# Performance work log

Hardware: AMD Instinct MI355X
Metric: run time of the kernel (lower is better)

The kernel has to match this reference:

```python
import jax, jax.numpy as jnp
import numpy as np
from jax import lax

D_MODEL = 768
BATCH = 16
SEQ = 2048
N_BLOCKS = D_MODEL // 3
LN_EPS = 1e-5


def setup_inputs() -> dict:
    key = jax.random.key(0)
    ks = jax.random.split(key, 4)
    scale = 1.0 / np.sqrt(D_MODEL)
    x = jax.random.normal(ks[0], (BATCH, SEQ, D_MODEL), dtype=jnp.float32)
    W_biv = jax.random.normal(ks[1], (D_MODEL, D_MODEL), dtype=jnp.float32) * scale
    b_biv = jnp.zeros((D_MODEL,), dtype=jnp.float32)
    W_decay = jax.random.normal(ks[2], (1, D_MODEL), dtype=jnp.float32) * scale
    b_decay = jnp.full((1,), 1.4, dtype=jnp.float32)  # nn.init.constant_(decay_proj.bias, 1.4)
    W_in = jax.random.normal(ks[3], (D_MODEL, D_MODEL), dtype=jnp.float32) * scale
    b_in = jnp.zeros((D_MODEL,), dtype=jnp.float32)
    ln_gamma = jnp.ones((D_MODEL,), dtype=jnp.float32)
    ln_beta = jnp.zeros((D_MODEL,), dtype=jnp.float32)
    return {"x": x, "W_biv": W_biv, "b_biv": b_biv, "W_decay": W_decay,
            "b_decay": b_decay, "W_in": W_in, "b_in": b_in,
            "ln_gamma": ln_gamma, "ln_beta": ln_beta}


def _quat_rotate_blocks(h_blocks, biv):
    """h_blocks, biv: (batch, n_blocks, 3) -> rotated (batch, n_blocks, 3)."""
    norm_b = jnp.maximum(jnp.linalg.norm(biv, axis=-1, keepdims=True), 1e-8)
    half = norm_b * 0.5
    w = jnp.cos(half)[..., 0]
    s = (jnp.sin(half) / norm_b)[..., 0]
    # note the original maps bivector components in reversed order
    qx = s * biv[..., 2]
    qy = -s * biv[..., 1]
    qz = s * biv[..., 0]
    vx, vy, vz = h_blocks[..., 0], h_blocks[..., 1], h_blocks[..., 2]
    tx = 2.0 * (qy * vz - qz * vy)
    ty = 2.0 * (qz * vx - qx * vz)
    tz = 2.0 * (qx * vy - qy * vx)
    rx = vx + w * tx + (qy * tz - qz * ty)
    ry = vy + w * ty + (qz * tx - qx * tz)
    rz = vz + w * tz + (qx * ty - qy * tx)
    return jnp.stack([rx, ry, rz], axis=-1)


def reference(x, W_biv, b_biv, W_decay, b_decay, W_in, b_in, ln_gamma, ln_beta):
    B, S, D = x.shape
    nb = D // 3
    # precompute all per-timestep projections as big GEMMs
    biv = (jnp.einsum('bsd,ed->bse', x, W_biv) + b_biv).reshape(B, S, nb, 3)
    decay = jax.nn.sigmoid(jnp.einsum('bsd,ed->bse', x, W_decay) + b_decay)  # (B,S,1)
    inj = jnp.einsum('bsd,ed->bse', x, W_in) + b_in  # (B,S,D)

    def step(h, t):
        biv_t, decay_t, inj_t = t
        rot = _quat_rotate_blocks(h.reshape(B, nb, 3), biv_t).reshape(B, D)
        h_next = decay_t * rot + inj_t
        return h_next, h_next

    xs = (jnp.moveaxis(biv, 1, 0), jnp.moveaxis(decay, 1, 0), jnp.moveaxis(inj, 1, 0))
    h0 = jnp.zeros((B, D), dtype=x.dtype)
    _, out = lax.scan(step, h0, xs)  # (S,B,D)
    out = jnp.moveaxis(out, 0, 1)  # (B,S,D)

    mean = jnp.mean(out, axis=-1, keepdims=True)
    var = jnp.mean(jnp.square(out - mean), axis=-1, keepdims=True)
    normed = (out - mean) * lax.rsqrt(var + LN_EPS) * ln_gamma + ln_beta
    return normed + x
```

## Files before the change

kernel.cpp:

```cpp
#include <hip/hip_runtime.h>
#include <stdint.h>

#define D_MODEL 768
#define BATCH   16
#define SEQ     2048
#define M_ROWS  (BATCH * SEQ)
#define LN_EPS  1e-5f

#define CHUNKS  64
#define CLEN    (SEQ / CHUNKS)
#define PFB     8

typedef __attribute__((ext_vector_type(4))) float        f32x4;
typedef __attribute__((ext_vector_type(8))) __bf16       bf16x8;
typedef __attribute__((ext_vector_type(2))) unsigned int u32x2;

__device__ __forceinline__ unsigned short f2bf(float f) {
    union { float f; uint32_t u; } v; v.f = f;
    uint32_t u = v.u;
    uint32_t r = (u + 0x7FFFu + ((u >> 16) & 1u)) >> 16;
    return (unsigned short)r;
}
__device__ __forceinline__ float bf2f(unsigned short u) {
    union { uint32_t u; float f; } v; v.u = (uint32_t)u << 16; return v.f;
}
__device__ __forceinline__ float bfx(u32x2 v, int k) {
    unsigned int w = (k & 2) ? v[1] : v[0];
    return bf2f((unsigned short)(w >> ((k & 1) * 16)));
}

__device__ __forceinline__ void gload_lds16(const void* g, void* l) {
    __builtin_amdgcn_global_load_lds(
        (const __attribute__((address_space(1))) unsigned int*)g,
        (__attribute__((address_space(3))) unsigned int*)l,
        16, 0, 0);
}

__global__ __launch_bounds__(256) void k_conv_decay(
    const float* __restrict__ x, const float* __restrict__ Wd,
    const float* __restrict__ bd, unsigned short* __restrict__ xb,
    float* __restrict__ decay)
{
    int row = blockIdx.x;
    int i   = threadIdx.x;
    const float* xr = x + (size_t)row * D_MODEL;
    float v0 = xr[i], v1 = xr[i + 256], v2 = xr[i + 512];
    unsigned short* xbr = xb + (size_t)row * D_MODEL;
    xbr[i] = f2bf(v0); xbr[i + 256] = f2bf(v1); xbr[i + 512] = f2bf(v2);

    float part = v0 * Wd[i] + v1 * Wd[i + 256] + v2 * Wd[i + 512];
    #pragma unroll
    for (int off = 32; off; off >>= 1) part += __shfl_down(part, off);
    __shared__ float wsum[4];
    int wid = i >> 6, lane = i & 63;
    if (lane == 0) wsum[wid] = part;
    __syncthreads();
    if (i == 0) {
        float s = wsum[0] + wsum[1] + wsum[2] + wsum[3] + bd[0];
        decay[row] = 1.f / (1.f + __expf(-s));
    }
}

__global__ __launch_bounds__(256) void k_conv_w(
    const float* __restrict__ Wb, const float* __restrict__ Wi,
    unsigned short* __restrict__ Wdst)
{
    const int NW = D_MODEL * D_MODEL;
    int g = blockIdx.x * 256 + threadIdx.x;
    int base = g * 4;
    unsigned short* dst = Wdst + base;
    const float* src;
    if (base < NW) { src = Wb + base; }
    else           { src = Wi + (base - NW); }
    float4 v = *(const float4*)src;
    ushort4 o;
    o.x = f2bf(v.x); o.y = f2bf(v.y); o.z = f2bf(v.z); o.w = f2bf(v.w);
    *(ushort4*)dst = o;
}

#define BM 128
#define BN 128
#define NBX 12

__global__ __launch_bounds__(256) void k_gemm_fused(
    const unsigned short* __restrict__ A,
    const unsigned short* __restrict__ Bw,
    const float* __restrict__ bias_biv, const float* __restrict__ bias_in,
    u32x2* __restrict__ bivq, u32x2* __restrict__ injq)
{
    const int K = D_MODEL;
    __shared__ unsigned short As[BM * 32];
    __shared__ unsigned short Bs[BN * 32];

    int id  = blockIdx.x;
    int swz = (id & 7) * (NBX * (M_ROWS / BM) / 8) + (id >> 3);
    int bxc = swz % NBX, byr = swz / NBX;
    int m0 = byr * BM, n0 = bxc * BN;

    int tid  = threadIdx.x;
    int wave = tid >> 6, lane = tid & 63;
    int wm = wave >> 1, wn = wave & 1;

    f32x4 acc[4][4] = {};

    for (int k0 = 0; k0 < K; k0 += 32) {
        #pragma unroll
        for (int hh = 0; hh < 2; ++hh) {
            int c  = wave * 128 + hh * 64 + lane;
            int r  = c >> 2;
            int sl = (c & 3) ^ ((r >> 1) & 3);
            gload_lds16(A  + (size_t)(m0 + r) * K + k0 + sl * 8, (char*)As + c * 16);
            gload_lds16(Bw + (size_t)(n0 + r) * K + k0 + sl * 8, (char*)Bs + c * 16);
        }
        __syncthreads();

        bf16x8 af[4], bfr[4];
        int kq = lane >> 4;
        int rl = lane & 15;
        #pragma unroll
        for (int i = 0; i < 4; ++i) {
            int ra = wm * 64 + i * 16 + rl;
            int ca = kq ^ ((ra >> 1) & 3);
            af[i]  = *reinterpret_cast<const bf16x8*>((const char*)As + ra * 64 + ca * 16);
            int rb = wn * 64 + i * 16 + rl;
            int cb = kq ^ ((rb >> 1) & 3);
            bfr[i] = *reinterpret_cast<const bf16x8*>((const char*)Bs + rb * 64 + cb * 16);
        }
        #pragma unroll
        for (int i = 0; i < 4; ++i)
            #pragma unroll
            for (int j = 0; j < 4; ++j)
                acc[i][j] = __builtin_amdgcn_mfma_f32_16x16x32_bf16(af[i], bfr[j], acc[i][j], 0, 0, 0);
        __syncthreads();
    }

    u32x2* Cq; const float* bias; int nloc;
    if (n0 < D_MODEL) { Cq = bivq; bias = bias_biv; nloc = n0; }
    else              { Cq = injq; bias = bias_in;  nloc = n0 - D_MODEL; }
    int cl = lane & 15;
    int q4 = lane >> 4;
    int rowq0 = (m0 + wm * 64) >> 2;
    #pragma unroll
    for (int j = 0; j < 4; ++j) {
        int col = nloc + wn * 64 + j * 16 + cl;
        float bs = bias[col];
        #pragma unroll
        for (int i = 0; i < 4; ++i) {
            f32x4 a = acc[i][j];
            unsigned int lo = (unsigned int)f2bf(a[0] + bs) | ((unsigned int)f2bf(a[1] + bs) << 16);
            unsigned int hi = (unsigned int)f2bf(a[2] + bs) | ((unsigned int)f2bf(a[3] + bs) << 16);
            size_t qi = (size_t)(rowq0 + i * 4 + q4) * D_MODEL + col;
            u32x2 pk = {lo, hi};
            Cq[qi] = pk;
        }
    }
}

#define QSTEP_CORE(BX,BY,BZ, IX,IY,IZ, DD)                              \
    {   float n2   = (BX)*(BX) + (BY)*(BY) + (BZ)*(BZ);                 \
        float nrm  = fmaxf(__builtin_sqrtf(n2), 1e-8f);                 \
        float half = 0.5f * nrm;                                        \
        float w = __cosf(half);                                         \
        float s = __sinf(half) / nrm;                                   \
        float qx = s * (BZ), qy = -s * (BY), qz = s * (BX);             \
        float tx = 2.f * (qy * hz - qz * hy);                           \
        float ty = 2.f * (qz * hx - qx * hz);                           \
        float tz = 2.f * (qx * hy - qy * hx);                           \
        float rx = hx + w * tx + (qy * tz - qz * ty);                   \
        float ry = hy + w * ty + (qz * tx - qx * tz);                   \
        float rz = hz + w * tz + (qx * ty - qy * tx);                   \
        hx = fmaf((DD), rx, (IX));                                      \
        hy = fmaf((DD), ry, (IY));                                      \
        hz = fmaf((DD), rz, (IZ));                                      \
        float nQw = w * Qw - qx * Qx - qy * Qy - qz * Qz;               \
        float nQx = w * Qx + Qw * qx + (qy * Qz - qz * Qy);             \
        float nQy = w * Qy + Qw * qy + (qz * Qx - qx * Qz);             \
        float nQz = w * Qz + Qw * qz + (qx * Qy - qy * Qx);             \
        Qw = nQw; Qx = nQx; Qy = nQy; Qz = nQz;                         \
        S *= (DD);                                                      \
    }

__global__ __launch_bounds__(256) void k_scan_p1(
    const u32x2* __restrict__ bivq, const u32x2* __restrict__ injq,
    const float* __restrict__ decay,
    float* __restrict__ ops)
{
    int j = threadIdx.x;
    int c = blockIdx.x & (CHUNKS - 1);
    int b = blockIdx.x >> 6;
    size_t qrow = ((size_t)b * SEQ + (size_t)c * CLEN) >> 2;
    const u32x2* bv = bivq + qrow * D_MODEL + 3 * j;
    const u32x2* ij = injq + qrow * D_MODEL + 3 * j;
    const float* dk = decay + (size_t)b * SEQ + c * CLEN;

    u32x2 Ab0, Ab1, Ab2, Ai0, Ai1, Ai2; f32x4 Ad;
    u32x2 Bb0, Bb1, Bb2, Bi0, Bi1, Bi2; f32x4 Bd;

    #define LOADQ1(P, q)                                                  \
        P##b0 = bv[(size_t)(q) * D_MODEL + 0];                            \
        P##b1 = bv[(size_t)(q) * D_MODEL + 1];                            \
        P##b2 = bv[(size_t)(q) * D_MODEL + 2];                            \
        P##i0 = ij[(size_t)(q) * D_MODEL + 0];                            \
        P##i1 = ij[(size_t)(q) * D_MODEL + 1];                            \
        P##i2 = ij[(size_t)(q) * D_MODEL + 2];                            \
        P##d  = *(const f32x4*)(dk + (q) * 4);

    #define PROC41(P)                                                     \
        _Pragma("unroll")                                                 \
        for (int k = 0; k < 4; ++k) {                                     \
            float bx = bfx(P##b0, k), by = bfx(P##b1, k), bz = bfx(P##b2, k); \
            float ix = bfx(P##i0, k), iy = bfx(P##i1, k), iz = bfx(P##i2, k); \
            float d = P##d[k];                                            \
            QSTEP_CORE(bx, by, bz, ix, iy, iz, d)                         \
        }

    float hx = 0.f, hy = 0.f, hz = 0.f;
    float Qw = 1.f, Qx = 0.f, Qy = 0.f, Qz = 0.f, S = 1.f;

    LOADQ1(A, 0)
    LOADQ1(B, 1)
    #pragma unroll
    for (int q0 = 0; q0 < CLEN / 4; q0 += 2) {
        PROC41(A)
        if (q0 + 2 < CLEN / 4) { LOADQ1(A, q0 + 2) }
        PROC41(B)
        if (q0 + 3 < CLEN / 4) { LOADQ1(B, q0 + 3) }
    }
    #undef LOADQ1
    #undef PROC41

    float* op = ops + ((size_t)(b * CHUNKS + c) * 256 + j) * 8;
    f32x4 o0 = {Qw, Qx, Qy, Qz};
    f32x4 o1 = {S, hx, hy, hz};
    *(f32x4*)op = o0;
    *(f32x4*)(op + 4) = o1;
}

__global__ __launch_bounds__(64) void k_scan_p2(
    const float* __restrict__ ops, float* __restrict__ hs)
{
    int gid = blockIdx.x * 64 + threadIdx.x;
    int j = gid & 255, b = gid >> 8;

    float q0[PFB], q1[PFB], q2[PFB], q3[PFB], sc[PFB], o0[PFB], o1[PFB], o2[PFB];
    #pragma unroll
    for (int p = 0; p < PFB; ++p) {
        const float* op = ops + ((size_t)(b * CHUNKS + p) * 256 + j) * 8;
        f32x4 a = *(const f32x4*)op, bb = *(const f32x4*)(op + 4);
        q0[p] = a[0]; q1[p] = a[1]; q2[p] = a[2]; q3[p] = a[3];
        sc[p] = bb[0]; o0[p] = bb[1]; o1[p] = bb[2]; o2[p] = bb[3];
    }
    float hx = 0.f, hy = 0.f, hz = 0.f;
    for (int c0 = 0; c0 < CHUNKS; c0 += PFB) {
        #pragma unroll
        for (int p = 0; p < PFB; ++p) {
            int c = c0 + p;
            float* h = hs + ((size_t)(b * CHUNKS + c) * 256 + j) * 3;
            h[0] = hx; h[1] = hy; h[2] = hz;
            float w = q0[p], qx = q1[p], qy = q2[p], qz = q3[p];
            float s = sc[p], bx = o0[p], by = o1[p], bz = o2[p];
            int cn = c + PFB;
            if (cn < CHUNKS) {
                const float* op = ops + ((size_t)(b * CHUNKS + cn) * 256 + j) * 8;
                f32x4 a = *(const f32x4*)op, bb = *(const f32x4*)(op + 4);
                q0[p] = a[0]; q1[p] = a[1]; q2[p] = a[2]; q3[p] = a[3];
                sc[p] = bb[0]; o0[p] = bb[1]; o1[p] = bb[2]; o2[p] = bb[3];
            }
            float tx = 2.f * (qy * hz - qz * hy);
            float ty = 2.f * (qz * hx - qx * hz);
            float tz = 2.f * (qx * hy - qy * hx);
            float rx = hx + w * tx + (qy * tz - qz * ty);
            float ry = hy + w * ty + (qz * tx - qx * tz);
            float rz = hz + w * tz + (qx * ty - qy * tx);
            hx = fmaf(s, rx, bx);
            hy = fmaf(s, ry, by);
            hz = fmaf(s, rz, bz);
        }
    }
}

__global__ __launch_bounds__(256) void k_scan_p3(
    const u32x2* __restrict__ bivq, const u32x2* __restrict__ injq,
    const float* __restrict__ decay, const float* __restrict__ hs,
    const float* __restrict__ x, const float* __restrict__ gamma,
    const float* __restrict__ beta, float* __restrict__ out)
{
    int blk = blockIdx.x;
    int c = blk & (CHUNKS - 1);
    int b = blk >> 6;
    int j = threadIdx.x;
    size_t rowbase = ((size_t)b * SEQ + (size_t)c * CLEN) * D_MODEL + (size_t)j * 3;
    size_t qrow    = ((size_t)b * SEQ + (size_t)c * CLEN) >> 2;
    const u32x2* bv = bivq + qrow * D_MODEL + 3 * j;
    const u32x2* ij = injq + qrow * D_MODEL + 3 * j;
    const float* xr = x   + rowbase;
    float*       po = out + rowbase;
    const float* dk = decay + (size_t)b * SEQ + c * CLEN;
    const float* h0 = hs + ((size_t)(b * CHUNKS + c) * 256 + j) * 3;
    float hx = h0[0], hy = h0[1], hz = h0[2];
    float Qw = 1.f, Qx = 0.f, Qy = 0.f, Qz = 0.f, S = 1.f;

    float g0 = gamma[j * 3], g1 = gamma[j * 3 + 1], g2 = gamma[j * 3 + 2];
    float e0 = beta[j * 3],  e1 = beta[j * 3 + 1],  e2 = beta[j * 3 + 2];

    __shared__ float sb[8];
    __shared__ float mv[2];
    int wid = j >> 6, lane = j & 63;

    u32x2 Ab0, Ab1, Ab2, Ai0, Ai1, Ai2; f32x4 Ad;
    float Ax0, Ax1, Ax2, Ax3, Ax4, Ax5, Ax6, Ax7, Ax8, Ax9, Ax10, Ax11;
    u32x2 Bb0, Bb1, Bb2, Bi0, Bi1, Bi2; f32x4 Bd;
    float Bx0, Bx1, Bx2, Bx3, Bx4, Bx5, Bx6, Bx7, Bx8, Bx9, Bx10, Bx11;

    #define LOADQ3(P, q)                                                  \
        P##b0 = bv[(size_t)(q) * D_MODEL + 0];                            \
        P##b1 = bv[(size_t)(q) * D_MODEL + 1];                            \
        P##b2 = bv[(size_t)(q) * D_MODEL + 2];                            \
        P##i0 = ij[(size_t)(q) * D_MODEL + 0];                            \
        P##i1 = ij[(size_t)(q) * D_MODEL + 1];                            \
        P##i2 = ij[(size_t)(q) * D_MODEL + 2];                            \
        P##d  = *(const f32x4*)(dk + (q) * 4);                            \
        P##x0  = xr[((size_t)(q) * 4 + 0) * D_MODEL + 0];                 \
        P##x1  = xr[((size_t)(q) * 4 + 0) * D_MODEL + 1];                 \
        P##x2  = xr[((size_t)(q) * 4 + 0) * D_MODEL + 2];                 \
        P##x3  = xr[((size_t)(q) * 4 + 1) * D_MODEL + 0];                 \
        P##x4  = xr[((size_t)(q) * 4 + 1) * D_MODEL + 1];                 \
        P##x5  = xr[((size_t)(q) * 4 + 1) * D_MODEL + 2];                 \
        P##x6  = xr[((size_t)(q) * 4 + 2) * D_MODEL + 0];                 \
        P##x7  = xr[((size_t)(q) * 4 + 2) * D_MODEL + 1];                 \
        P##x8  = xr[((size_t)(q) * 4 + 2) * D_MODEL + 2];                 \
        P##x9  = xr[((size_t)(q) * 4 + 3) * D_MODEL + 0];                 \
        P##x10 = xr[((size_t)(q) * 4 + 3) * D_MODEL + 1];                 \
        P##x11 = xr[((size_t)(q) * 4 + 3) * D_MODEL + 2];

    #define STEP3(P, k, T)                                                \
    {   float bx = bfx(P##b0, k), by = bfx(P##b1, k), bz = bfx(P##b2, k); \
        float ix = bfx(P##i0, k), iy = bfx(P##i1, k), iz = bfx(P##i2, k); \
        float d = P##d[k];                                                \
        QSTEP_CORE(bx, by, bz, ix, iy, iz, d)                             \
        float sp = hx + hy + hz;                                          \
        float qp = hx * hx + hy * hy + hz * hz;                           \
        _Pragma("unroll")                                                 \
        for (int off = 32; off; off >>= 1) {                              \
            sp += __shfl_down(sp, off);                                   \
            qp += __shfl_down(qp, off);                                   \
        }                                                                 \
        if (lane == 0) { sb[wid] = sp; sb[wid + 4] = qp; }                \
        __syncthreads();                                                  \
        if (j == 0) {                                                     \
            float Ssum = sb[0] + sb[1] + sb[2] + sb[3];                   \
            float Qsum = sb[4] + sb[5] + sb[6] + sb[7];                   \
            float mean = Ssum * (1.f / 768.f);                            \
            float var  = Qsum * (1.f / 768.f) - mean * mean;              \
            mv[0] = mean; mv[1] = rsqrtf(var + LN_EPS);                   \
        }                                                                 \
        __syncthreads();                                                  \
        float mean = mv[0], rstd = mv[1];                                 \
        float* o2 = po + (size_t)(T) * D_MODEL;                           \
        o2[0] = (hx - mean) * rstd * g0 + e0 + P##x##0j(k, 0);            \
        o2[1] = (hy - mean) * rstd * g1 + e1 + P##x##0j(k, 1);            \
        o2[2] = (hz - mean) * rstd * g2 + e2 + P##x##0j(k, 2);            \
    }

    #define PROC43(P, QBASE)                                              \
    {   { float xa = P##x0,  xbv = P##x1,  xc = P##x2;                    \
          STEP3X(P, 0, (QBASE) * 4 + 0, xa, xbv, xc) }                    \
        { float xa = P##x3,  xbv = P##x4,  xc = P##x5;                    \
          STEP3X(P, 1, (QBASE) * 4 + 1, xa, xbv, xc) }                    \
        { float xa = P##x6,  xbv = P##x7,  xc = P##x8;                    \
          STEP3X(P, 2, (QBASE) * 4 + 2, xa, xbv, xc) }                    \
        { float xa = P##x9,  xbv = P##x10, xc = P##x11;                   \
          STEP3X(P, 3, (QBASE) * 4 + 3, xa, xbv, xc) }                    \
    }

    #define STEP3X(P, k, T, XA, XB, XC)                                   \
    {   float bx = bfx(P##b0, k), by = bfx(P##b1, k), bz = bfx(P##b2, k); \
        float ix = bfx(P##i0, k), iy = bfx(P##i1, k), iz = bfx(P##i2, k); \
        float d = P##d[k];                                                \
        QSTEP_CORE(bx, by, bz, ix, iy, iz, d)                             \
        float sp = hx + hy + hz;                                          \
        float qp = hx * hx + hy * hy + hz * hz;                           \
        _Pragma("unroll")                                                 \
        for (int off = 32; off; off >>= 1) {                              \
            sp += __shfl_down(sp, off);                                   \
            qp += __shfl_down(qp, off);                                   \
        }                                                                 \
        if (lane == 0) { sb[wid] = sp; sb[wid + 4] = qp; }                \
        __syncthreads();                                                  \
        if (j == 0) {                                                     \
            float Ssum = sb[0] + sb[1] + sb[2] + sb[3];                   \
            float Qsum = sb[4] + sb[5] + sb[6] + sb[7];                   \
            float mean = Ssum * (1.f / 768.f);                            \
            float var  = Qsum * (1.f / 768.f) - mean * mean;              \
            mv[0] = mean; mv[1] = rsqrtf(var + LN_EPS);                   \
        }                                                                 \
        __syncthreads();                                                  \
        float mean = mv[0], rstd = mv[1];                                 \
        float* o2 = po + (size_t)(T) * D_MODEL;                           \
        o2[0] = (hx - mean) * rstd * g0 + e0 + (XA);                      \
        o2[1] = (hy - mean) * rstd * g1 + e1 + (XB);                      \
        o2[2] = (hz - mean) * rstd * g2 + e2 + (XC);                      \
    }

    LOADQ3(A, 0)
    LOADQ3(B, 1)
    #pragma unroll
    for (int q0 = 0; q0 < CLEN / 4; q0 += 2) {
        PROC43(A, q0)
        if (q0 + 2 < CLEN / 4) { LOADQ3(A, q0 + 2) }
        PROC43(B, q0 + 1)
        if (q0 + 3 < CLEN / 4) { LOADQ3(B, q0 + 3) }
    }
    (void)Qw; (void)Qx; (void)Qy; (void)Qz; (void)S;
}

extern "C" void kernel_launch(void* const* d_in, const int* in_sizes, int n_in,
                              void* d_out, int out_size, void* d_ws, size_t ws_size,
                              hipStream_t stream) {
    const float* x     = (const float*)d_in[0];
    const float* W_biv = (const float*)d_in[1];
    const float* b_biv = (const float*)d_in[2];
    const float* W_dec = (const float*)d_in[3];
    const float* b_dec = (const float*)d_in[4];
    const float* W_in  = (const float*)d_in[5];
    const float* b_in  = (const float*)d_in[6];
    const float* gamma = (const float*)d_in[7];
    const float* beta  = (const float*)d_in[8];
    float* out = (float*)d_out;

    char* ws = (char*)d_ws;
    unsigned short* xb    = (unsigned short*)(ws);
    unsigned short* Wcat  = (unsigned short*)(ws + 50331648);
    float*          decay = (float*)         (ws + 52690944);
    u32x2*          bivq  = (u32x2*)         (ws + 52822016);
    u32x2*          injq  = (u32x2*)         (ws + 103153664);
    float*          ops   = (float*)(ws);
    float*          hs    = (float*)(ws + 8388608);

    (void)in_sizes; (void)n_in; (void)out_size; (void)ws_size;

    k_conv_decay<<<M_ROWS, 256, 0, stream>>>(x, W_dec, b_dec, xb, decay);
    k_conv_w    <<<1152,   256, 0, stream>>>(W_biv, W_in, Wcat);
    k_gemm_fused<<<NBX * (M_ROWS / BM), 256, 0, stream>>>(xb, Wcat, b_biv, b_in, bivq, injq);
    k_scan_p1   <<<1024, 256, 0, stream>>>(bivq, injq, decay, ops);
    k_scan_p2   <<<64,   64,  0, stream>>>(ops, hs);
    k_scan_p3   <<<1024, 256, 0, stream>>>(bivq, injq, decay, hs, x, gamma, beta, out);
}
```

Baseline: 232.5 us.

## Rewrite fused GEMM with 256x256 tiles and double-buffered async LDS pipeline

Replaces the 128x128, 256-thread GEMM with a 256x256-tile, 512-thread kernel. It double-buffers K=64 stages in 128KB of dynamic LDS, issuing global-to-LDS loads for future half-stages while MFMAs run on the current one. Explicit vmcnt waits, raw s_barrier and setprio control the overlap. The goal is more data reuse per tile and hidden load latency, at the cost of heavy LDS use and far fewer blocks (768), which may limit occupancy and cause tail imbalance. An unused STEP3 macro is also removed.

```diff
diff --git a/kernel.cpp b/kernel.cpp
--- a/kernel.cpp
+++ b/kernel.cpp
@@ -78,80 +78,109 @@
     *(ushort4*)dst = o;
 }
 
-#define BM 128
-#define BN 128
-#define NBX 12
-
-__global__ __launch_bounds__(256) void k_gemm_fused(
+#define GBM 256
+#define GBN 256
+#define GNBX 6
+#define GNBY 128
+#define NT   12
+
+__global__ __launch_bounds__(512, 2) void k_gemm_fused(
     const unsigned short* __restrict__ A,
     const unsigned short* __restrict__ Bw,
     const float* __restrict__ bias_biv, const float* __restrict__ bias_in,
     u32x2* __restrict__ bivq, u32x2* __restrict__ injq)
 {
-    const int K = D_MODEL;
-    __shared__ unsigned short As[BM * 32];
-    __shared__ unsigned short Bs[BN * 32];
+    extern __shared__ unsigned short LDSBUF[];
+    unsigned short* LA = LDSBUF;
+    unsigned short* LB = LDSBUF + 32768;
 
     int id  = blockIdx.x;
-    int swz = (id & 7) * (NBX * (M_ROWS / BM) / 8) + (id >> 3);
-    int bxc = swz % NBX, byr = swz / NBX;
-    int m0 = byr * BM, n0 = bxc * BN;
+    int swz = (id & 7) * 96 + (id >> 3);
+    int bxc = swz % GNBX, byr = swz / GNBX;
+    int m0 = byr * GBM, n0 = bxc * GBN;
 
     int tid  = threadIdx.x;
-    int wave = tid >> 6, lane = tid & 63;
-    int wm = wave >> 1, wn = wave & 1;
-
-    f32x4 acc[4][4] = {};
-
-    for (int k0 = 0; k0 < K; k0 += 32) {
-        #pragma unroll
-        for (int hh = 0; hh < 2; ++hh) {
-            int c  = wave * 128 + hh * 64 + lane;
-            int r  = c >> 2;
-            int sl = (c & 3) ^ ((r >> 1) & 3);
-            gload_lds16(A  + (size_t)(m0 + r) * K + k0 + sl * 8, (char*)As + c * 16);
-            gload_lds16(Bw + (size_t)(n0 + r) * K + k0 + sl * 8, (char*)Bs + c * 16);
-        }
-        __syncthreads();
-
-        bf16x8 af[4], bfr[4];
-        int kq = lane >> 4;
-        int rl = lane & 15;
-        #pragma unroll
-        for (int i = 0; i < 4; ++i) {
-            int ra = wm * 64 + i * 16 + rl;
-            int ca = kq ^ ((ra >> 1) & 3);
-            af[i]  = *reinterpret_cast<const bf16x8*>((const char*)As + ra * 64 + ca * 16);
-            int rb = wn * 64 + i * 16 + rl;
-            int cb = kq ^ ((rb >> 1) & 3);
-            bfr[i] = *reinterpret_cast<const bf16x8*>((const char*)Bs + rb * 64 + cb * 16);
-        }
-        #pragma unroll
-        for (int i = 0; i < 4; ++i)
-            #pragma unroll
-            for (int j = 0; j < 4; ++j)
-                acc[i][j] = __builtin_amdgcn_mfma_f32_16x16x32_bf16(af[i], bfr[j], acc[i][j], 0, 0, 0);
-        __syncthreads();
-    }
+    int wid  = tid >> 6, lane = tid & 63;
+    int wm = wid >> 2, wn = wid & 3;
+    int rl = lane & 15, kq = lane >> 4;
+    int sl = kq ^ ((rl >> 1) & 3);
+    int aoff = (wm * 128 + rl) * 32 + sl * 8;
+    int boff = (wn * 64  + rl) * 32 + sl * 8;
+
+    f32x4 acc[8][4] = {};
+
+    #define STAGE_HALF(DBUF, KT, HH) do {                                        \
+        _Pragma("unroll")                                                        \
+        for (int p = 0; p < 2; ++p) {                                            \
+            int idx = p * 512 + tid;                                             \
+            int row = idx >> 2;                                                  \
+            int ss  = ((idx & 3) ^ ((idx >> 3) & 3)) * 8;  \
+            gload_lds16(A  + (size_t)(m0 + row) * D_MODEL + (KT) * 64 + (HH) * 32 + ss, \
+                        LA + (DBUF) * 16384 + (HH) * 8192 + idx * 8);            \
+            gload_lds16(Bw + (size_t)(n0 + row) * D_MODEL + (KT) * 64 + (HH) * 32 + ss, \
+                        LB + (DBUF) * 16384 + (HH) * 8192 + idx * 8);            \
+        }                                                                        \
+    } while (0)
+
+    #define PHASE(D, H, DOSTAGE, SBUF, SKT, SHH, WAITSTR) do {                   \
+        bf16x8 af[8], bfv[4];                                                    \
+        const unsigned short* pa = LA + (D) * 16384 + (H) * 8192 + aoff;         \
+        const unsigned short* pb = LB + (D) * 16384 + (H) * 8192 + boff;         \
+        _Pragma("unroll")                                                        \
+        for (int i = 0; i < 8; ++i) af[i]  = *(const bf16x8*)(pa + i * 512);     \
+        _Pragma("unroll")                                                        \
+        for (int j = 0; j < 4; ++j) bfv[j] = *(const bf16x8*)(pb + j * 512);     \
+        if (DOSTAGE) STAGE_HALF(SBUF, SKT, SHH);                                 \
+        asm volatile(WAITSTR ::: "memory");                                      \
+        asm volatile("s_barrier" ::: "memory");                                  \
+        asm volatile("s_waitcnt lgkmcnt(0)" ::: "memory");                       \
+        __builtin_amdgcn_sched_barrier(0);                                       \
+        __builtin_amdgcn_s_setprio(1);                                           \
+        _Pragma("unroll")                                                        \
+        for (int i = 0; i < 8; ++i)                                              \
+            _Pragma("unroll")                                                    \
+            for (int j = 0; j < 4; ++j)                                          \
+                acc[i][j] = __builtin_amdgcn_mfma_f32_16x16x32_bf16(             \
+                    af[i], bfv[j], acc[i][j], 0, 0, 0);                          \
+        __builtin_amdgcn_s_setprio(0);                                           \
+        asm volatile("s_barrier" ::: "memory");                                  \
+    } while (0)
+
+    STAGE_HALF(0, 0, 0);
+    STAGE_HALF(0, 0, 1);
+    STAGE_HALF(1, 1, 0);
+    asm volatile("s_waitcnt vmcnt(8)" ::: "memory");
+    asm volatile("s_barrier" ::: "memory");
+
+    for (int t = 0; t < 10; ++t) {
+        int cur = t & 1;
+        PHASE(cur, 0, true, cur ^ 1, t + 1, 1, "s_waitcnt vmcnt(8)");
+        PHASE(cur, 1, true, cur,     t + 2, 0, "s_waitcnt vmcnt(8)");
+    }
+    PHASE(0, 0, true,  1, 11, 1, "s_waitcnt vmcnt(8)");
+    PHASE(0, 1, false, 0, 0,  0, "s_waitcnt vmcnt(4)");
+    PHASE(1, 0, false, 0, 0,  0, "s_waitcnt vmcnt(0)");
+    PHASE(1, 1, false, 0, 0,  0, "");
+
+    #undef PHASE
+    #undef STAGE_HALF
 
     u32x2* Cq; const float* bias; int nloc;
     if (n0 < D_MODEL) { Cq = bivq; bias = bias_biv; nloc = n0; }
     else              { Cq = injq; bias = bias_in;  nloc = n0 - D_MODEL; }
     int cl = lane & 15;
-    int q4 = lane >> 4;
-    int rowq0 = (m0 + wm * 64) >> 2;
+    int qbase = (m0 >> 2) + wm * 32 + (lane >> 4);
     #pragma unroll
     for (int j = 0; j < 4; ++j) {
         int col = nloc + wn * 64 + j * 16 + cl;
         float bs = bias[col];
         #pragma unroll
-        for (int i = 0; i < 4; ++i) {
+        for (int i = 0; i < 8; ++i) {
             f32x4 a = acc[i][j];
             unsigned int lo = (unsigned int)f2bf(a[0] + bs) | ((unsigned int)f2bf(a[1] + bs) << 16);
             unsigned int hi = (unsigned int)f2bf(a[2] + bs) | ((unsigned int)f2bf(a[3] + bs) << 16);
-            size_t qi = (size_t)(rowq0 + i * 4 + q4) * D_MODEL + col;
             u32x2 pk = {lo, hi};
-            Cq[qi] = pk;
+            Cq[(size_t)(qbase + i * 4) * D_MODEL + col] = pk;
         }
     }
 }
@@ -332,35 +361,6 @@
         P##x9  = xr[((size_t)(q) * 4 + 3) * D_MODEL + 0];                 \
         P##x10 = xr[((size_t)(q) * 4 + 3) * D_MODEL + 1];                 \
         P##x11 = xr[((size_t)(q) * 4 + 3) * D_MODEL + 2];
-
-    #define STEP3(P, k, T)                                                \
-    {   float bx = bfx(P##b0, k), by = bfx(P##b1, k), bz = bfx(P##b2, k); \
-        float ix = bfx(P##i0, k), iy = bfx(P##i1, k), iz = bfx(P##i2, k); \
-        float d = P##d[k];                                                \
-        QSTEP_CORE(bx, by, bz, ix, iy, iz, d)                             \
-        float sp = hx + hy + hz;                                          \
-        float qp = hx * hx + hy * hy + hz * hz;                           \
-        _Pragma("unroll")                                                 \
-        for (int off = 32; off; off >>= 1) {                              \
-            sp += __shfl_down(sp, off);                                   \
-            qp += __shfl_down(qp, off);                                   \
-        }                                                                 \
-        if (lane == 0) { sb[wid] = sp; sb[wid + 4] = qp; }                \
-        __syncthreads();                                                  \
-        if (j == 0) {                                                     \
-            float Ssum = sb[0] + sb[1] + sb[2] + sb[3];                   \
-            float Qsum = sb[4] + sb[5] + sb[6] + sb[7];                   \
-            float mean = Ssum * (1.f / 768.f);                            \
-            float var  = Qsum * (1.f / 768.f) - mean * mean;              \
-            mv[0] = mean; mv[1] = rsqrtf(var + LN_EPS);                   \
-        }                                                                 \
-        __syncthreads();                                                  \
-        float mean = mv[0], rstd = mv[1];                                 \
-        float* o2 = po + (size_t)(T) * D_MODEL;                           \
-        o2[0] = (hx - mean) * rstd * g0 + e0 + P##x##0j(k, 0);            \
-        o2[1] = (hy - mean) * rstd * g1 + e1 + P##x##0j(k, 1);            \
-        o2[2] = (hz - mean) * rstd * g2 + e2 + P##x##0j(k, 2);            \
-    }
 
     #define PROC43(P, QBASE)                                              \
     {   { float xa = P##x0,  xbv = P##x1,  xc = P##x2;                    \
@@ -439,9 +439,12 @@
 
     (void)in_sizes; (void)n_in; (void)out_size; (void)ws_size;
 
+    hipFuncSetAttribute((const void*)k_gemm_fused,
+                        hipFuncAttributeMaxDynamicSharedMemorySize, 131072);
+
     k_conv_decay<<<M_ROWS, 256, 0, stream>>>(x, W_dec, b_dec, xb, decay);
     k_conv_w    <<<1152,   256, 0, stream>>>(W_biv, W_in, Wcat);
-    k_gemm_fused<<<NBX * (M_ROWS / BM), 256, 0, stream>>>(xb, Wcat, b_biv, b_in, bivq, injq);
+    k_gemm_fused<<<GNBX * GNBY, 512, 131072, stream>>>(xb, Wcat, b_biv, b_in, bivq, injq);
     k_scan_p1   <<<1024, 256, 0, stream>>>(bivq, injq, decay, ops);
     k_scan_p2   <<<64,   64,  0, stream>>>(ops, hs);
     k_scan_p3   <<<1024, 256, 0, stream>>>(bivq, injq, decay, hs, x, gamma, beta, out);
```

Result: faster. 220.1 us (-5.3%).
